# Performance work log

Measured on AMD Instinct MI355X. Metric: run time of the kernel, lower is better.

Reference implementation:

```python
import jax, jax.numpy as jnp
import numpy as np

B, K, D = 8, 4000, 256
H, DQ, DV = 8, 32, 32
WIN, PAD = 200, 50
STEP = WIN - 2 * PAD  # 100
BETA = 0.25


def setup_inputs() -> dict:
    key = jax.random.key(0)
    ks = jax.random.split(key, 14)
    s = 0.02
    return {
        "query": jax.random.normal(ks[0], (B, K, D), jnp.float32),
        "key": jax.random.normal(ks[1], (B, K, D), jnp.float32),
        "value": jax.random.normal(ks[2], (B, K, D), jnp.float32),
        "Wq": jax.random.normal(ks[3], (D, H * DQ), jnp.float32) * s,
        "bq": jax.random.normal(ks[4], (H * DQ,), jnp.float32) * s,
        "Wk": jax.random.normal(ks[5], (D, H * DQ), jnp.float32) * s,
        "bk": jax.random.normal(ks[6], (H * DQ,), jnp.float32) * s,
        "Wv": jax.random.normal(ks[7], (D, H * DV), jnp.float32) * s,
        "bv": jax.random.normal(ks[8], (H * DV,), jnp.float32) * s,
        "Wo": jax.random.normal(ks[9], (H * DV, D), jnp.float32) * s,
        "bo": jax.random.normal(ks[10], (D,), jnp.float32) * s,
    }


def _windows(x, n_win):
    starts = jnp.arange(n_win) * STEP
    idx = starts[:, None] + jnp.arange(WIN)[None, :]
    return x[:, :, idx, :]


def reference(query, key, value, Wq, bq, Wk, bk, Wv, bv, Wo, bo):
    b, k_len, d = query.shape
    pad = lambda t: jnp.pad(t, ((0, 0), (PAD, PAD), (0, 0)), mode='edge')  # replicate pad
    qp, kp, vp = pad(query), pad(key), pad(value)
    kpad = k_len + 2 * PAD
    n_win = (kpad - WIN) // STEP + 1

    def proj(x, Wm, bias, dh):
        y = x @ Wm + bias                       # [B, Kp, H*dh]
        return y.reshape(b, kpad, H, dh).transpose(0, 2, 1, 3)  # [B, H, Kp, dh]

    q = _windows(proj(qp, Wq, bq, DQ), n_win)
    kk = _windows(proj(kp, Wk, bk, DQ), n_win)
    v = _windows(proj(vp, Wv, bv, DV), n_win)

    scores = jnp.einsum('bhnid,bhnjd->bhnij', q, kk) / jnp.sqrt(jnp.float32(WIN))
    dist = jnp.abs(jnp.arange(WIN)[:, None] - jnp.arange(WIN)[None, :]).astype(scores.dtype)
    cauchy = (1.0 / (1.0 + BETA * dist * dist)) * (1.0 - jnp.eye(WIN, dtype=scores.dtype))
    scores = scores * cauchy
    causal = jnp.triu(jnp.ones((WIN, WIN), dtype=bool), k=1)  # attention_size is not None -> causal masking
    scores = jnp.where(causal, -jnp.inf, scores)
    attn = jax.nn.softmax(scores, axis=-1)
    out = jnp.einsum('bhnij,bhnjd->bhnid', attn, v)
    out = out[:, :, :, PAD:WIN - PAD, :].reshape(b, H, k_len, DV)
    out = out.transpose(0, 2, 1, 3).reshape(b, k_len, H * DV)  # heads concatenated, head-major slices
    return out @ Wo + bo
```

## Files before the change

### kernel.cpp

```cpp
#include <hip/hip_runtime.h>


typedef __bf16 bf16_t;
typedef __bf16 bf16x8 __attribute__((ext_vector_type(8)));
typedef float  f32x4  __attribute__((ext_vector_type(4)));

#define MFMA16(a, b, c) __builtin_amdgcn_mfma_f32_16x16x32_bf16((a), (b), (c), 0, 0, 0)

typedef __attribute__((address_space(1))) const unsigned char gas_u8;
typedef __attribute__((address_space(3))) unsigned char las_u8;

static __device__ __forceinline__ void gload16(const void* g, void* l) {
  __builtin_amdgcn_global_load_lds((gas_u8*)g, (las_u8*)l, 16, 0, 0);
}

static __device__ __forceinline__ bf16x8 cvt8(float4 a, float4 b) {
  bf16x8 r;
  r[0] = (bf16_t)a.x; r[1] = (bf16_t)a.y; r[2] = (bf16_t)a.z; r[3] = (bf16_t)a.w;
  r[4] = (bf16_t)b.x; r[5] = (bf16_t)b.y; r[6] = (bf16_t)b.z; r[7] = (bf16_t)b.w;
  return r;
}

static __device__ __forceinline__ unsigned short bbits(bf16_t v) {
  union { bf16_t b; unsigned short u; } c; c.b = v; return c.u;
}

__global__ __launch_bounds__(256)
void prep_weights(const float* __restrict__ Wq, const float* __restrict__ Wk,
                  const float* __restrict__ Wv, const float* __restrict__ Wo,
                  bf16_t* __restrict__ wt) {
  const int mat  = blockIdx.x >> 6;
  const int tile = blockIdx.x & 63;
  const int kt = (tile >> 3) * 32, nt = (tile & 7) * 32;
  const float* W = (mat == 0) ? Wq : (mat == 1) ? Wk : (mat == 2) ? Wv : Wo;
  __shared__ float t[32][33];
  const int tx = threadIdx.x & 31, ty = threadIdx.x >> 5;
#pragma unroll
  for (int i = 0; i < 32; i += 8)
    t[ty + i][tx] = W[(size_t)(kt + ty + i) * 256 + nt + tx];
  __syncthreads();
  bf16_t* dst = wt + (size_t)mat * 65536;
#pragma unroll
  for (int i = 0; i < 32; i += 8)
    dst[(size_t)(nt + ty + i) * 256 + kt + tx] = (bf16_t)t[tx][ty + i];
}

__global__ __launch_bounds__(256)
void proj_gemm(const float* __restrict__ qx, const float* __restrict__ kx,
               const float* __restrict__ vx, const bf16_t* __restrict__ wt,
               const float* __restrict__ bq, const float* __restrict__ bk,
               const float* __restrict__ bv,
               bf16_t* __restrict__ qb, bf16_t* __restrict__ kb,
               bf16_t* __restrict__ vt, int M, float qscale) {
  const int mode = blockIdx.y;
  const float* X    = (mode == 0) ? qx : (mode == 1) ? kx : vx;
  const float* bias = (mode == 0) ? bq : (mode == 1) ? bk : bv;
  const bf16_t* W   = wt + (size_t)mode * 65536;

  __shared__ __align__(16) char lds[2 * 24576];

  const int tid  = threadIdx.x;
  const int lane = tid & 63;
  const int w    = tid >> 6;
  const int lo   = lane & 15, hi = lane >> 4;
  const int m0   = blockIdx.x * 64;

  const float* asrc[2];
  int aoff[2];
#pragma unroll
  for (int j = 0; j < 2; ++j) {
    const int s = (w * 2 + j) * 64 + lane;
    const int row = s >> 3, f = s & 7;
    const int ar = (m0 + row < M) ? (m0 + row) : (M - 1);
    asrc[j] = X + (size_t)ar * 256 + ((f ^ (row & 7)) << 2);
    aoff[j] = (w * 2 + j) * 1024;
  }
  const bf16_t* bsrc[4];
  int boff[4];
#pragma unroll
  for (int j = 0; j < 4; ++j) {
    const int s = (w * 4 + j) * 64 + lane;
    bsrc[j] = W + (size_t)(s >> 2) * 256 + ((s & 3) << 3);
    boff[j] = 8192 + (w * 4 + j) * 1024;
  }
  int abase[4], bbase[4];
#pragma unroll
  for (int mi = 0; mi < 4; ++mi)
    abase[mi] = (((mi * 16 + lo) << 3) + ((2 * hi) ^ (lo & 7))) << 4;
#pragma unroll
  for (int ni = 0; ni < 4; ++ni)
    bbase[ni] = 8192 + (w * 64 + ni * 16 + lo) * 64 + hi * 16;

  f32x4 acc[4][4] = {};

#pragma unroll
  for (int j = 0; j < 2; ++j) gload16(asrc[j], lds + aoff[j]);
#pragma unroll
  for (int j = 0; j < 4; ++j) gload16(bsrc[j], lds + boff[j]);

  for (int t = 0; t < 8; ++t) {
    const int cur = (t & 1) * 24576;
    if (t < 7) {
      const int nxt = ((t + 1) & 1) * 24576;
#pragma unroll
      for (int j = 0; j < 2; ++j) gload16(asrc[j] + (t + 1) * 32, lds + nxt + aoff[j]);
#pragma unroll
      for (int j = 0; j < 4; ++j) gload16(bsrc[j] + (t + 1) * 32, lds + nxt + boff[j]);
      asm volatile("s_waitcnt vmcnt(6)" ::: "memory");
    } else {
      asm volatile("s_waitcnt vmcnt(0)" ::: "memory");
    }
    __builtin_amdgcn_sched_barrier(0);
    __builtin_amdgcn_s_barrier();

    bf16x8 af[4], bfv[4];
#pragma unroll
    for (int mi = 0; mi < 4; ++mi) {
      const float4 v0 = *(const float4*)(lds + cur + abase[mi]);
      const float4 v1 = *(const float4*)(lds + cur + (abase[mi] ^ 16));
      af[mi] = cvt8(v0, v1);
    }
#pragma unroll
    for (int ni = 0; ni < 4; ++ni)
      bfv[ni] = *(const bf16x8*)(lds + cur + bbase[ni]);
#pragma unroll
    for (int mi = 0; mi < 4; ++mi)
#pragma unroll
      for (int ni = 0; ni < 4; ++ni)
        acc[mi][ni] = MFMA16(af[mi], bfv[ni], acc[mi][ni]);
    __builtin_amdgcn_sched_barrier(0);
    __builtin_amdgcn_s_barrier();
  }

#pragma unroll
  for (int mi = 0; mi < 4; ++mi) {
    const int mb = m0 + mi * 16 + hi * 4;
    if (mb >= M) continue;
#pragma unroll
    for (int ni = 0; ni < 4; ++ni) {
      const int n = w * 64 + ni * 16 + lo;
      const float bia = bias[n];
      if (mode == 0) {
#pragma unroll
        for (int rr = 0; rr < 4; ++rr)
          qb[(size_t)(mb + rr) * 256 + n] = (bf16_t)((acc[mi][ni][rr] + bia) * qscale);
      } else if (mode == 1) {
        const int b = mb / 4000, t = mb - b * 4000;
#pragma unroll
        for (int rr = 0; rr < 4; ++rr)
          kb[((size_t)b * 4064 + t + 50 + rr) * 256 + n] = (bf16_t)(acc[mi][ni][rr] + bia);
      } else {
        const int b = mb / 4000, t = mb - b * 4000;
        const int h = n >> 5, dv = n & 31;
        bf16_t* O = vt + ((size_t)((b * 8 + h) * 32 + dv)) * 4064 + t + 50;
        unsigned short e0 = bbits((bf16_t)(acc[mi][ni][0] + bia));
        unsigned short e1 = bbits((bf16_t)(acc[mi][ni][1] + bia));
        unsigned short e2 = bbits((bf16_t)(acc[mi][ni][2] + bia));
        unsigned short e3 = bbits((bf16_t)(acc[mi][ni][3] + bia));
        unsigned* O32 = (unsigned*)O;
        O32[0] = (unsigned)e0 | ((unsigned)e1 << 16);
        O32[1] = (unsigned)e2 | ((unsigned)e3 << 16);
      }
    }
  }
}

__global__ __launch_bounds__(256)
void out_gemm(const bf16_t* __restrict__ ao, const bf16_t* __restrict__ wt,
              const float* __restrict__ bias, float* __restrict__ Out, int M) {
  __shared__ __align__(16) char lds[2 * 20480];

  const int tid  = threadIdx.x;
  const int lane = tid & 63;
  const int w    = tid >> 6;
  const int lo   = lane & 15, hi = lane >> 4;
  const int m0   = blockIdx.x * 64;

  const bf16_t* asrc;
  int aoff;
  {
    const int s = w * 64 + lane;
    const int row = s >> 2;
    const int ar = (m0 + row < M) ? (m0 + row) : (M - 1);
    asrc = ao + (size_t)ar * 256 + ((s & 3) << 3);
    aoff = w * 1024;
  }
  const bf16_t* bsrc[4];
  int boff[4];
#pragma unroll
  for (int j = 0; j < 4; ++j) {
    const int s = (w * 4 + j) * 64 + lane;
    bsrc[j] = wt + (size_t)(s >> 2) * 256 + ((s & 3) << 3);
    boff[j] = 4096 + (w * 4 + j) * 1024;
  }
  int abase[4], bbase[4];
#pragma unroll
  for (int mi = 0; mi < 4; ++mi)
    abase[mi] = (mi * 16 + lo) * 64 + hi * 16;
#pragma unroll
  for (int ni = 0; ni < 4; ++ni)
    bbase[ni] = 4096 + (w * 64 + ni * 16 + lo) * 64 + hi * 16;

  f32x4 acc[4][4] = {};

  gload16(asrc, lds + aoff);
#pragma unroll
  for (int j = 0; j < 4; ++j) gload16(bsrc[j], lds + boff[j]);

  for (int t = 0; t < 8; ++t) {
    const int cur = (t & 1) * 20480;
    if (t < 7) {
      const int nxt = ((t + 1) & 1) * 20480;
      gload16(asrc + (t + 1) * 32, lds + nxt + aoff);
#pragma unroll
      for (int j = 0; j < 4; ++j) gload16(bsrc[j] + (t + 1) * 32, lds + nxt + boff[j]);
      asm volatile("s_waitcnt vmcnt(5)" ::: "memory");
    } else {
      asm volatile("s_waitcnt vmcnt(0)" ::: "memory");
    }
    __builtin_amdgcn_sched_barrier(0);
    __builtin_amdgcn_s_barrier();

    bf16x8 af[4], bfv[4];
#pragma unroll
    for (int mi = 0; mi < 4; ++mi)
      af[mi] = *(const bf16x8*)(lds + cur + abase[mi]);
#pragma unroll
    for (int ni = 0; ni < 4; ++ni)
      bfv[ni] = *(const bf16x8*)(lds + cur + bbase[ni]);
#pragma unroll
    for (int mi = 0; mi < 4; ++mi)
#pragma unroll
      for (int ni = 0; ni < 4; ++ni)
        acc[mi][ni] = MFMA16(af[mi], bfv[ni], acc[mi][ni]);
    __builtin_amdgcn_sched_barrier(0);
    __builtin_amdgcn_s_barrier();
  }

#pragma unroll
  for (int mi = 0; mi < 4; ++mi) {
    const int mb = m0 + mi * 16 + hi * 4;
    if (mb >= M) continue;
#pragma unroll
    for (int ni = 0; ni < 4; ++ni) {
      const int n = w * 64 + ni * 16 + lo;
      const float bia = bias[n];
#pragma unroll
      for (int rr = 0; rr < 4; ++rr)
        Out[(size_t)(mb + rr) * 256 + n] = acc[mi][ni][rr] + bia;
    }
  }
}

__global__ void fill_edges(bf16_t* __restrict__ kb, bf16_t* __restrict__ vt, int nb) {
  const int idx = blockIdx.x * 256 + threadIdx.x;
  const int kcnt = nb * 64 * 256;
  if (idx < kcnt) {
    const int b  = idx >> 14;
    const int pp = (idx >> 8) & 63;
    const int nn = idx & 255;
    const int p  = (pp < 50) ? pp : pp + 4000;
    bf16_t v = (pp < 50) ? kb[((size_t)b * 4064 + 50) * 256 + nn] : (bf16_t)0.f;
    kb[((size_t)b * 4064 + p) * 256 + nn] = v;
  } else {
    const int j  = idx - kcnt;
    const int bh = j >> 11;
    const int dv = (j >> 6) & 31;
    const int pp = j & 63;
    const int p  = (pp < 50) ? pp : pp + 4000;
    bf16_t v = (pp < 50) ? vt[((size_t)bh * 32 + dv) * 4064 + 50] : (bf16_t)0.f;
    vt[((size_t)bh * 32 + dv) * 4064 + p] = v;
  }
}

__global__ __launch_bounds__(448)
void attn_win(const bf16_t* __restrict__ qb, const bf16_t* __restrict__ kb,
              const bf16_t* __restrict__ vt, bf16_t* __restrict__ ao) {
  const int blk = blockIdx.x;
  const int n = blk % 40;
  const int h = (blk / 40) & 7;
  const int b = blk / 320;
  const int wv = threadIdx.x >> 6;
  const int lane = threadIdx.x & 63;
  const int lo = lane & 15, hi = lane >> 4;

  __shared__ __align__(16) bf16_t E[7][16][40];

  const int i0 = 50 + 16 * wv;
  int jtmax = (65 + 16 * wv) >> 4;
  if (jtmax > 9) jtmax = 9;
  const int reach = jtmax * 16 + 16;

  int tq = n * 100 + 16 * wv + lo;
  if (tq > 3999) tq = 3999;
  const bf16x8 qf = *(const bf16x8*)&qb[((size_t)b * 4000 + tq) * 256 + h * 32 + hi * 8];

  const f32x4 zero = {0.f, 0.f, 0.f, 0.f};
  bf16x8 onesf;
#pragma unroll
  for (int u = 0; u < 8; ++u) onesf[u] = (bf16_t)1.0f;

  f32x4 o0 = zero, o1 = zero, sm = zero;
  const size_t vbase = ((size_t)((b * 8 + h) * 32)) * 4064 + n * 100;
  const size_t kbase = ((size_t)(b * 4064 + n * 100)) * 256 + h * 32 + hi * 8;
  const int dbase = i0 + hi * 4 - lo;

#pragma unroll
  for (int kt = 0; kt < 5; ++kt) if (kt * 32 < reach) {
#pragma unroll
    for (int half = 0; half < 2; ++half) {
      const int jt = kt * 2 + half;
      if (jt <= jtmax) {
        const bf16x8 kf = *(const bf16x8*)&kb[kbase + (size_t)(jt * 16 + lo) * 256];
        const f32x4 s = MFMA16(qf, kf, zero);
#pragma unroll
        for (int r = 0; r < 4; ++r) {
          const int d = dbase + r - jt * 16;
          const float df = (float)d;
          float c = __builtin_amdgcn_rcpf(__builtin_fmaf(0.25f * df, df, 1.f));
          c = (d == 0) ? 0.f : c;
          float e = __expf(s[r] * c);
          e = (d < 0) ? 0.f : e;
          E[wv][hi * 4 + r][half * 16 + lo] = (bf16_t)e;
        }
      } else {
#pragma unroll
        for (int r = 0; r < 4; ++r)
          E[wv][hi * 4 + r][half * 16 + lo] = (bf16_t)0.f;
      }
    }
    const bf16x8 pf = *(const bf16x8*)&E[wv][lo][hi * 8];
    const bf16x8 v0 = *(const bf16x8*)&vt[vbase + (size_t)lo * 4064 + kt * 32 + hi * 8];
    const bf16x8 v1 = *(const bf16x8*)&vt[vbase + (size_t)(16 + lo) * 4064 + kt * 32 + hi * 8];
    o0 = MFMA16(pf, v0, o0);
    o1 = MFMA16(pf, v1, o1);
    sm = MFMA16(pf, onesf, sm);
  }

#pragma unroll
  for (int r = 0; r < 4; ++r) {
    const int i = i0 + hi * 4 + r;
    if (i < 150) {
      const float ri = __builtin_amdgcn_rcpf(sm[r]);
      const int t = n * 100 + i - 50;
      bf16_t* op = &ao[((size_t)b * 4000 + t) * 256 + h * 32];
      op[lo]      = (bf16_t)(o0[r] * ri);
      op[16 + lo] = (bf16_t)(o1[r] * ri);
    }
  }
}

extern "C" void kernel_launch(void* const* d_in, const int* in_sizes, int n_in,
                              void* d_out, int out_size, void* d_ws, size_t ws_size,
                              hipStream_t stream) {
  (void)in_sizes; (void)n_in; (void)out_size;
  const float* query = (const float*)d_in[0];
  const float* key   = (const float*)d_in[1];
  const float* value = (const float*)d_in[2];
  const float* Wq = (const float*)d_in[3];
  const float* bq = (const float*)d_in[4];
  const float* Wk = (const float*)d_in[5];
  const float* bk = (const float*)d_in[6];
  const float* Wv = (const float*)d_in[7];
  const float* bv = (const float*)d_in[8];
  const float* Wo = (const float*)d_in[9];
  const float* bo = (const float*)d_in[10];

  int bc = 8;
  while (bc > 1 && 524288ull + (unsigned long long)bc * 8257536ull > (unsigned long long)ws_size)
    bc >>= 1;

  bf16_t* wt = (bf16_t*)d_ws;
  bf16_t* qb = wt + 4 * 65536;
  bf16_t* kb = qb + (size_t)bc * 4000 * 256;
  bf16_t* vt = kb + (size_t)bc * 4064 * 256;
  bf16_t* ao = vt + (size_t)bc * 8 * 32 * 4064;

  prep_weights<<<256, 256, 0, stream>>>(Wq, Wk, Wv, Wo, wt);

  const float qscale = 0.07071067811865475f;

  for (int b0 = 0; b0 < 8; b0 += bc) {
    const int M = bc * 4000;
    const int mblk = (M + 63) / 64;
    const float* qx = query + (size_t)b0 * 4000 * 256;
    const float* kx = key   + (size_t)b0 * 4000 * 256;
    const float* vx = value + (size_t)b0 * 4000 * 256;
    float* ox = (float*)d_out + (size_t)b0 * 4000 * 256;

    proj_gemm<<<dim3(mblk, 3), 256, 0, stream>>>(qx, kx, vx, wt, bq, bk, bv,
                                                 qb, kb, vt, M, qscale);
    fill_edges<<<bc * 128, 256, 0, stream>>>(kb, vt, bc);
    attn_win<<<bc * 320, 448, 0, stream>>>(qb, kb, vt, ao);
    out_gemm<<<dim3(mblk), 256, 0, stream>>>(ao, wt + 3 * 65536, bo, ox, M);
  }
}
```

Measured before the change: 94.29 us.

## Preload whole A tile as bf16 in LDS and fold edge padding into projection

```diff
diff --git a/kernel.cpp b/kernel.cpp
--- a/kernel.cpp
+++ b/kernel.cpp
@@ -2,6 +2,7 @@
 
 
 typedef __bf16 bf16_t;
+typedef __bf16 bf16x4 __attribute__((ext_vector_type(4)));
 typedef __bf16 bf16x8 __attribute__((ext_vector_type(8)));
 typedef float  f32x4  __attribute__((ext_vector_type(4)));
 
@@ -14,16 +15,18 @@
   __builtin_amdgcn_global_load_lds((gas_u8*)g, (las_u8*)l, 16, 0, 0);
 }
 
-static __device__ __forceinline__ bf16x8 cvt8(float4 a, float4 b) {
-  bf16x8 r;
+static __device__ __forceinline__ bf16x4 cvt4(float4 a) {
+  bf16x4 r;
   r[0] = (bf16_t)a.x; r[1] = (bf16_t)a.y; r[2] = (bf16_t)a.z; r[3] = (bf16_t)a.w;
-  r[4] = (bf16_t)b.x; r[5] = (bf16_t)b.y; r[6] = (bf16_t)b.z; r[7] = (bf16_t)b.w;
   return r;
 }
 
 static __device__ __forceinline__ unsigned short bbits(bf16_t v) {
   union { bf16_t b; unsigned short u; } c; c.b = v; return c.u;
 }
+
+#define APITCH 264
+#define ABYTES (64 * APITCH * 2)
 
 __global__ __launch_bounds__(256)
 void prep_weights(const float* __restrict__ Wq, const float* __restrict__ Wk,
@@ -57,7 +60,9 @@
   const float* bias = (mode == 0) ? bq : (mode == 1) ? bk : bv;
   const bf16_t* W   = wt + (size_t)mode * 65536;
 
-  __shared__ __align__(16) char lds[2 * 24576];
+  __shared__ __align__(16) char lds[ABYTES + 2 * 16384];
+  bf16_t* laA = (bf16_t*)lds;
+  char*   ldsB = lds + ABYTES;
 
   const int tid  = threadIdx.x;
   const int lane = tid & 63;
@@ -65,48 +70,44 @@
   const int lo   = lane & 15, hi = lane >> 4;
   const int m0   = blockIdx.x * 64;
 
-  const float* asrc[2];
-  int aoff[2];
-#pragma unroll
-  for (int j = 0; j < 2; ++j) {
-    const int s = (w * 2 + j) * 64 + lane;
-    const int row = s >> 3, f = s & 7;
-    const int ar = (m0 + row < M) ? (m0 + row) : (M - 1);
-    asrc[j] = X + (size_t)ar * 256 + ((f ^ (row & 7)) << 2);
-    aoff[j] = (w * 2 + j) * 1024;
-  }
+  {
+    const int colq = (tid & 63) * 4;
+    const int r0   = tid >> 6;
+#pragma unroll
+    for (int u = 0; u < 16; ++u) {
+      const int r = r0 + u * 4;
+      int ar = m0 + r; if (ar >= M) ar = M - 1;
+      const float4 v = *(const float4*)(X + (size_t)ar * 256 + colq);
+      *(bf16x4*)&laA[r * APITCH + colq] = cvt4(v);
+    }
+  }
+
   const bf16_t* bsrc[4];
   int boff[4];
 #pragma unroll
   for (int j = 0; j < 4; ++j) {
     const int s = (w * 4 + j) * 64 + lane;
     bsrc[j] = W + (size_t)(s >> 2) * 256 + ((s & 3) << 3);
-    boff[j] = 8192 + (w * 4 + j) * 1024;
-  }
-  int abase[4], bbase[4];
-#pragma unroll
-  for (int mi = 0; mi < 4; ++mi)
-    abase[mi] = (((mi * 16 + lo) << 3) + ((2 * hi) ^ (lo & 7))) << 4;
+    boff[j] = (w * 4 + j) * 1024;
+  }
+  int bbase[4];
 #pragma unroll
   for (int ni = 0; ni < 4; ++ni)
-    bbase[ni] = 8192 + (w * 64 + ni * 16 + lo) * 64 + hi * 16;
+    bbase[ni] = (w * 64 + ni * 16 + lo) * 64 + hi * 16;
+
+#pragma unroll
+  for (int j = 0; j < 4; ++j) gload16(bsrc[j], ldsB + boff[j]);
+  __syncthreads();
 
   f32x4 acc[4][4] = {};
 
-#pragma unroll
-  for (int j = 0; j < 2; ++j) gload16(asrc[j], lds + aoff[j]);
-#pragma unroll
-  for (int j = 0; j < 4; ++j) gload16(bsrc[j], lds + boff[j]);
-
   for (int t = 0; t < 8; ++t) {
-    const int cur = (t & 1) * 24576;
+    const int cur = (t & 1) * 16384;
     if (t < 7) {
-      const int nxt = ((t + 1) & 1) * 24576;
-#pragma unroll
-      for (int j = 0; j < 2; ++j) gload16(asrc[j] + (t + 1) * 32, lds + nxt + aoff[j]);
-#pragma unroll
-      for (int j = 0; j < 4; ++j) gload16(bsrc[j] + (t + 1) * 32, lds + nxt + boff[j]);
-      asm volatile("s_waitcnt vmcnt(6)" ::: "memory");
+      const int nxt = ((t + 1) & 1) * 16384;
+#pragma unroll
+      for (int j = 0; j < 4; ++j) gload16(bsrc[j] + (t + 1) * 32, ldsB + nxt + boff[j]);
+      asm volatile("s_waitcnt vmcnt(4)" ::: "memory");
     } else {
       asm volatile("s_waitcnt vmcnt(0)" ::: "memory");
     }
@@ -115,14 +116,11 @@
 
     bf16x8 af[4], bfv[4];
 #pragma unroll
-    for (int mi = 0; mi < 4; ++mi) {
-      const float4 v0 = *(const float4*)(lds + cur + abase[mi]);
-      const float4 v1 = *(const float4*)(lds + cur + (abase[mi] ^ 16));
-      af[mi] = cvt8(v0, v1);
-    }
+    for (int mi = 0; mi < 4; ++mi)
+      af[mi] = *(const bf16x8*)&laA[(mi * 16 + lo) * APITCH + t * 32 + hi * 8];
 #pragma unroll
     for (int ni = 0; ni < 4; ++ni)
-      bfv[ni] = *(const bf16x8*)(lds + cur + bbase[ni]);
+      bfv[ni] = *(const bf16x8*)(ldsB + cur + bbase[ni]);
 #pragma unroll
     for (int mi = 0; mi < 4; ++mi)
 #pragma unroll
@@ -147,19 +145,30 @@
       } else if (mode == 1) {
         const int b = mb / 4000, t = mb - b * 4000;
 #pragma unroll
-        for (int rr = 0; rr < 4; ++rr)
-          kb[((size_t)b * 4064 + t + 50 + rr) * 256 + n] = (bf16_t)(acc[mi][ni][rr] + bia);
+        for (int rr = 0; rr < 4; ++rr) {
+          const bf16_t v = (bf16_t)(acc[mi][ni][rr] + bia);
+          kb[((size_t)b * 4064 + t + 50 + rr) * 256 + n] = v;
+          if (t == 0 && rr == 0)
+            for (int p = 0; p < 50; ++p)
+              kb[((size_t)b * 4064 + p) * 256 + n] = v;
+        }
       } else {
         const int b = mb / 4000, t = mb - b * 4000;
         const int h = n >> 5, dv = n & 31;
-        bf16_t* O = vt + ((size_t)((b * 8 + h) * 32 + dv)) * 4064 + t + 50;
+        const size_t vrow = ((size_t)((b * 8 + h) * 32 + dv)) * 4064;
         unsigned short e0 = bbits((bf16_t)(acc[mi][ni][0] + bia));
         unsigned short e1 = bbits((bf16_t)(acc[mi][ni][1] + bia));
         unsigned short e2 = bbits((bf16_t)(acc[mi][ni][2] + bia));
         unsigned short e3 = bbits((bf16_t)(acc[mi][ni][3] + bia));
-        unsigned* O32 = (unsigned*)O;
+        unsigned* O32 = (unsigned*)(vt + vrow + t + 50);
         O32[0] = (unsigned)e0 | ((unsigned)e1 << 16);
         O32[1] = (unsigned)e2 | ((unsigned)e3 << 16);
+        if (t == 0) {
+          const unsigned vv = (unsigned)e0 | ((unsigned)e0 << 16);
+          unsigned* P = (unsigned*)(vt + vrow);
+#pragma unroll
+          for (int p = 0; p < 25; ++p) P[p] = vv;
+        }
       }
     }
   }
@@ -168,7 +177,9 @@
 __global__ __launch_bounds__(256)
 void out_gemm(const bf16_t* __restrict__ ao, const bf16_t* __restrict__ wt,
               const float* __restrict__ bias, float* __restrict__ Out, int M) {
-  __shared__ __align__(16) char lds[2 * 20480];
+  __shared__ __align__(16) char lds[ABYTES + 2 * 16384];
+  bf16_t* laA = (bf16_t*)lds;
+  char*   ldsB = lds + ABYTES;
 
   const int tid  = threadIdx.x;
   const int lane = tid & 63;
@@ -176,45 +187,44 @@
   const int lo   = lane & 15, hi = lane >> 4;
   const int m0   = blockIdx.x * 64;
 
-  const bf16_t* asrc;
-  int aoff;
   {
-    const int s = w * 64 + lane;
-    const int row = s >> 2;
-    const int ar = (m0 + row < M) ? (m0 + row) : (M - 1);
-    asrc = ao + (size_t)ar * 256 + ((s & 3) << 3);
-    aoff = w * 1024;
-  }
+    const int colb = (tid & 31) * 8;
+    const int r0   = tid >> 5;
+#pragma unroll
+    for (int u = 0; u < 8; ++u) {
+      const int r = r0 + u * 8;
+      int ar = m0 + r; if (ar >= M) ar = M - 1;
+      const bf16x8 v = *(const bf16x8*)(ao + (size_t)ar * 256 + colb);
+      *(bf16x8*)&laA[r * APITCH + colb] = v;
+    }
+  }
+
   const bf16_t* bsrc[4];
   int boff[4];
 #pragma unroll
   for (int j = 0; j < 4; ++j) {
     const int s = (w * 4 + j) * 64 + lane;
     bsrc[j] = wt + (size_t)(s >> 2) * 256 + ((s & 3) << 3);
-    boff[j] = 4096 + (w * 4 + j) * 1024;
-  }
-  int abase[4], bbase[4];
-#pragma unroll
-  for (int mi = 0; mi < 4; ++mi)
-    abase[mi] = (mi * 16 + lo) * 64 + hi * 16;
+    boff[j] = (w * 4 + j) * 1024;
+  }
+  int bbase[4];
 #pragma unroll
   for (int ni = 0; ni < 4; ++ni)
-    bbase[ni] = 4096 + (w * 64 + ni * 16 + lo) * 64 + hi * 16;
+    bbase[ni] = (w * 64 + ni * 16 + lo) * 64 + hi * 16;
+
+#pragma unroll
+  for (int j = 0; j < 4; ++j) gload16(bsrc[j], ldsB + boff[j]);
+  __syncthreads();
 
   f32x4 acc[4][4] = {};
 
-  gload16(asrc, lds + aoff);
-#pragma unroll
-  for (int j = 0; j < 4; ++j) gload16(bsrc[j], lds + boff[j]);
-
   for (int t = 0; t < 8; ++t) {
-    const int cur = (t & 1) * 20480;
+    const int cur = (t & 1) * 16384;
     if (t < 7) {
-      const int nxt = ((t + 1) & 1) * 20480;
-      gload16(asrc + (t + 1) * 32, lds + nxt + aoff);
-#pragma unroll
-      for (int j = 0; j < 4; ++j) gload16(bsrc[j] + (t + 1) * 32, lds + nxt + boff[j]);
-      asm volatile("s_waitcnt vmcnt(5)" ::: "memory");
+      const int nxt = ((t + 1) & 1) * 16384;
+#pragma unroll
+      for (int j = 0; j < 4; ++j) gload16(bsrc[j] + (t + 1) * 32, ldsB + nxt + boff[j]);
+      asm volatile("s_waitcnt vmcnt(4)" ::: "memory");
     } else {
       asm volatile("s_waitcnt vmcnt(0)" ::: "memory");
     }
@@ -224,10 +234,10 @@
     bf16x8 af[4], bfv[4];
 #pragma unroll
     for (int mi = 0; mi < 4; ++mi)
-      af[mi] = *(const bf16x8*)(lds + cur + abase[mi]);
+      af[mi] = *(const bf16x8*)&laA[(mi * 16 + lo) * APITCH + t * 32 + hi * 8];
 #pragma unroll
     for (int ni = 0; ni < 4; ++ni)
-      bfv[ni] = *(const bf16x8*)(lds + cur + bbase[ni]);
+      bfv[ni] = *(const bf16x8*)(ldsB + cur + bbase[ni]);
 #pragma unroll
     for (int mi = 0; mi < 4; ++mi)
 #pragma unroll
@@ -249,27 +259,6 @@
       for (int rr = 0; rr < 4; ++rr)
         Out[(size_t)(mb + rr) * 256 + n] = acc[mi][ni][rr] + bia;
     }
-  }
-}
-
-__global__ void fill_edges(bf16_t* __restrict__ kb, bf16_t* __restrict__ vt, int nb) {
-  const int idx = blockIdx.x * 256 + threadIdx.x;
-  const int kcnt = nb * 64 * 256;
-  if (idx < kcnt) {
-    const int b  = idx >> 14;
-    const int pp = (idx >> 8) & 63;
-    const int nn = idx & 255;
-    const int p  = (pp < 50) ? pp : pp + 4000;
-    bf16_t v = (pp < 50) ? kb[((size_t)b * 4064 + 50) * 256 + nn] : (bf16_t)0.f;
-    kb[((size_t)b * 4064 + p) * 256 + nn] = v;
-  } else {
-    const int j  = idx - kcnt;
-    const int bh = j >> 11;
-    const int dv = (j >> 6) & 31;
-    const int pp = j & 63;
-    const int p  = (pp < 50) ? pp : pp + 4000;
-    bf16_t v = (pp < 50) ? vt[((size_t)bh * 32 + dv) * 4064 + 50] : (bf16_t)0.f;
-    vt[((size_t)bh * 32 + dv) * 4064 + p] = v;
   }
 }
 
@@ -390,7 +379,6 @@
 
     proj_gemm<<<dim3(mblk, 3), 256, 0, stream>>>(qx, kx, vx, wt, bq, bk, bv,
                                                  qb, kb, vt, M, qscale);
-    fill_edges<<<bc * 128, 256, 0, stream>>>(kb, vt, bc);
     attn_win<<<bc * 320, 448, 0, stream>>>(qb, kb, vt, ao);
     out_gemm<<<dim3(mblk), 256, 0, stream>>>(ao, wt + 3 * 65536, bo, ox, M);
   }
```

Measured after the change: 99.69 us. 1.06x slower.
